# Kernel optimization log

Hardware: AMD Instinct MI355X
Metric: run time of the kernel (lower is better)

Reference implementation:

```python
import jax, jax.numpy as jnp
import numpy as np

N_NODES = 50000
N_EDGES = 800000
NUM_FEATS = 128
HIDDEN = 512
OUT = 2


def setup_inputs() -> dict:
    key = jax.random.key(0)
    k1, k2, k3, k4 = jax.random.split(key, 4)
    X = jax.random.normal(k1, (N_NODES, NUM_FEATS), dtype=jnp.float32)
    edge_index = jax.random.randint(k2, (2, N_EDGES), 0, N_NODES, dtype=jnp.int64)
    W1 = jax.random.normal(k3, (NUM_FEATS, HIDDEN), dtype=jnp.float32) / np.sqrt(NUM_FEATS)
    b1 = jnp.zeros((HIDDEN,), dtype=jnp.float32)
    W2 = jax.random.normal(k4, (HIDDEN, OUT), dtype=jnp.float32) / np.sqrt(HIDDEN)
    b2 = jnp.zeros((OUT,), dtype=jnp.float32)
    return {"X": X, "edge_index": edge_index, "W1": W1, "b1": b1, "W2": W2, "b2": b2}


def _gcn_conv(x, W, b, src, dst, dinv, n):
    # PyG GCNConv: x' = D^{-1/2} (A + I) D^{-1/2} (x W) + b
    xw = x @ W  # [N, C]
    edge_norm = dinv[src] * dinv[dst]  # [E]
    msg = xw[src] * edge_norm[:, None]  # [E, C] gathered messages
    agg = jax.ops.segment_sum(msg, dst, num_segments=n)
    agg = agg + xw * (dinv * dinv)[:, None]  # self-loop contribution
    return agg + b


def reference(X, edge_index, W1, b1, W2, b2):
    n = X.shape[0]
    src, dst = edge_index[0], edge_index[1]
    # degree with self-loops (gcn_norm): deg[i] = in_degree(i) + 1
    deg = jax.ops.segment_sum(jnp.ones_like(dst, dtype=X.dtype), dst, num_segments=n) + 1.0
    dinv = jax.lax.rsqrt(deg)
    h = jax.nn.relu(_gcn_conv(X, W1, b1, src, dst, dinv, n))
    logits = _gcn_conv(h, W2, b2, src, dst, dinv, n)
    # nn.Softmax() on a 2D tensor defaults to dim=1
    return jax.nn.softmax(logits, axis=1)
```

## Files before the change

### kernel.cpp

```cpp
#include <hip/hip_runtime.h>

#define N_FEATS 128
#define HIDDEN 512
#define NPAD 50176
#define NBKT 196
#define SLAB 4608
#define PA_EPB 4096
#define PA_BLOCKS 196
#define XQ_BLOCKS 3125

typedef __attribute__((ext_vector_type(4))) float floatx4;
typedef __attribute__((ext_vector_type(8))) short shortx8;

__device__ __forceinline__ unsigned short f2bf(float f) {
    union { float f; unsigned u; } a; a.f = f;
    unsigned r = a.u + 0x7fff + ((a.u >> 16) & 1);
    return (unsigned short)(r >> 16);
}

__global__ __launch_bounds__(256) void k_initA(const float* __restrict__ W1,
        unsigned short* __restrict__ w1t, const float* __restrict__ X,
        signed char* __restrict__ Xq, float* __restrict__ scale,
        const int* __restrict__ src, const int* __restrict__ dst,
        int* __restrict__ bcur, unsigned* __restrict__ staging, int E, int N) {
    int b = blockIdx.x, tid = threadIdx.x;
    if (b < PA_BLOCKS) {
        __shared__ int hist[NBKT];
        __shared__ int base[NBKT];
        for (int i = tid; i < NBKT; i += 256) hist[i] = 0;
        __syncthreads();
        #pragma unroll
        for (int i = 0; i < 4; ++i) {
            int e = b * PA_EPB + (i * 256 + tid) * 4;
            if (e + 3 < E) {
                int4 d4 = *reinterpret_cast<const int4*>(dst + e);
                atomicAdd(&hist[d4.x >> 8], 1);
                atomicAdd(&hist[d4.y >> 8], 1);
                atomicAdd(&hist[d4.z >> 8], 1);
                atomicAdd(&hist[d4.w >> 8], 1);
            } else {
                for (int k = 0; k < 4; ++k)
                    if (e + k < E) atomicAdd(&hist[dst[e + k] >> 8], 1);
            }
        }
        __syncthreads();
        for (int i = tid; i < NBKT; i += 256) {
            int c = hist[i];
            base[i] = c ? atomicAdd(&bcur[i], c) : 0;
            hist[i] = 0;
        }
        __syncthreads();
        #pragma unroll
        for (int i = 0; i < 4; ++i) {
            int e = b * PA_EPB + (i * 256 + tid) * 4;
            if (e + 3 < E) {
                int4 d4 = *reinterpret_cast<const int4*>(dst + e);
                int4 s4 = *reinterpret_cast<const int4*>(src + e);
                #define PUT(dd, ss) { int bk = (dd) >> 8; int r = atomicAdd(&hist[bk], 1); \
                    int pos = base[bk] + r; if (pos < SLAB) \
                    staging[(size_t)bk * SLAB + pos] = ((unsigned)(ss) << 8) | (unsigned)((dd) & 255); }
                PUT(d4.x, s4.x) PUT(d4.y, s4.y) PUT(d4.z, s4.z) PUT(d4.w, s4.w)
            } else {
                for (int k = 0; k < 4; ++k)
                    if (e + k < E) { int dd = dst[e + k], ss = src[e + k]; PUT(dd, ss) }
                #undef PUT
            }
        }
    } else if (b < PA_BLOCKS + 16) {
        __shared__ unsigned short t[64][65];
        int bb = b - PA_BLOCKS;
        int ki = bb >> 3, ni = bb & 7;
        #pragma unroll
        for (int i = 0; i < 16; ++i) {
            int idx = tid + i * 256;
            int r = idx >> 6, c = idx & 63;
            t[r][c] = f2bf(W1[(ki * 64 + r) * 512 + ni * 64 + c]);
        }
        __syncthreads();
        #pragma unroll
        for (int i = 0; i < 16; ++i) {
            int idx = tid + i * 256;
            int rn = idx >> 6, ck = idx & 63;
            w1t[(ni * 64 + rn) * 128 + ki * 64 + ck] = t[ck][rn];
        }
    } else {
        int r = (b - PA_BLOCKS - 16) * 16 + (tid >> 4);
        int lane = tid & 15;
        if (r < N) {
            const float* xp = X + (size_t)r * N_FEATS + lane * 8;
            float4 v0 = *reinterpret_cast<const float4*>(xp);
            float4 v1 = *reinterpret_cast<const float4*>(xp + 4);
            float f[8] = {v0.x, v0.y, v0.z, v0.w, v1.x, v1.y, v1.z, v1.w};
            float mx = 0.f;
            #pragma unroll
            for (int k = 0; k < 8; ++k) mx = fmaxf(mx, fabsf(f[k]));
            #pragma unroll
            for (int off = 1; off < 16; off <<= 1) mx = fmaxf(mx, __shfl_xor(mx, off));
            float rs = (mx > 0.f) ? 127.0f / mx : 0.f;
            union { signed char c[8]; uint2 u; } o;
            #pragma unroll
            for (int k = 0; k < 8; ++k) {
                int q = (int)rintf(f[k] * rs);
                q = q > 127 ? 127 : (q < -127 ? -127 : q);
                o.c[k] = (signed char)q;
            }
            *reinterpret_cast<uint2*>(Xq + (size_t)r * N_FEATS + lane * 8) = o.u;
            if (lane == 0) scale[r] = (mx > 0.f) ? mx / 127.0f : 0.f;
        }
    }
}

__global__ __launch_bounds__(256) void k_bucketB(const int* __restrict__ bcur,
        const unsigned* __restrict__ staging, const float* __restrict__ scale,
        int* __restrict__ csr_g, int* __restrict__ offs_g,
        int* __restrict__ cursor, float* __restrict__ dinvs, float* __restrict__ dscale) {
    __shared__ int hist[256];
    __shared__ int offs_l[256];
    __shared__ int sc[256];
    int b = blockIdx.x, tid = threadIdx.x;
    hist[tid] = 0;
    __syncthreads();
    int cnt = bcur[b];
    if (cnt > SLAB) cnt = SLAB;
    const unsigned* st = staging + (size_t)b * SLAB;
    for (int j = tid; j < cnt; j += 256) atomicAdd(&hist[st[j] & 255u], 1);
    __syncthreads();
    int c = hist[tid];
    sc[tid] = c;
    __syncthreads();
    #pragma unroll
    for (int off = 1; off < 256; off <<= 1) {
        int t = (tid >= off) ? sc[tid - off] : 0;
        __syncthreads();
        sc[tid] += t;
        __syncthreads();
    }
    int excl = sc[tid] - c;
    offs_l[tid] = excl;
    int node = (b << 8) + tid;
    float dv = rsqrtf((float)c + 1.0f);
    cursor[node] = c;
    dinvs[node] = dv;
    dscale[node] = dv * scale[node];
    offs_g[node] = b * SLAB + excl;
    hist[tid] = 0;
    __syncthreads();
    for (int j = tid; j < cnt; j += 256) {
        unsigned v = st[j];
        int dl = (int)(v & 255u);
        int s = (int)(v >> 8);
        int p = atomicAdd(&hist[dl], 1);
        csr_g[b * SLAB + offs_l[dl] + p] = s;
    }
}

__global__ __launch_bounds__(512, 4) void k_gather_gemm(
        const int* __restrict__ cursor, const float* __restrict__ dinvs,
        const float* __restrict__ dscale, const int* __restrict__ offs_g,
        const int* __restrict__ csr_g, const signed char* __restrict__ Xq,
        const unsigned short* __restrict__ w1t, const float* __restrict__ b1,
        const float* __restrict__ W2, float2* __restrict__ lps, int N) {
    __shared__ unsigned short As[128][136];
    __shared__ unsigned short Bs[128][136];
    __shared__ float b1s[HIDDEN];
    __shared__ float W2s[HIDDEN * 2];

    const int tid = threadIdx.x;
    const int m0 = blockIdx.x * 128;
    for (int i = tid; i < HIDDEN; i += 512) b1s[i] = b1[i];
    for (int i = tid; i < HIDDEN * 2; i += 512) W2s[i] = W2[i];

    union Q8 { uint2 u; signed char c[8]; };

    const int lane16 = tid & 15;
    const int nsub = tid >> 4;
    #pragma unroll
    for (int h = 0; h < 4; ++h) {
        int r = h * 32 + nsub;
        int gm = m0 + r;
        if (gm < N) {
            float dv = dinvs[gm];
            float ds = dscale[gm];
            int beg = offs_g[gm];
            int cnt = cursor[gm];
            const signed char* xrow = Xq + (size_t)gm * N_FEATS + lane16 * 8;
            Q8 sv; sv.u = *reinterpret_cast<const uint2*>(xrow);
            float a[8];
            #pragma unroll
            for (int k = 0; k < 8; ++k) a[k] = ds * (float)sv.c[k];
            const int* cp = csr_g + beg;
            int j = 0;
            int4 nxt;
            if (cnt >= 4) nxt = *reinterpret_cast<const int4*>(cp);
            for (; j + 4 <= cnt; j += 4) {
                int4 s4 = nxt;
                if (j + 8 <= cnt) nxt = *reinterpret_cast<const int4*>(cp + j + 4);
                float w0 = dscale[s4.x], w1 = dscale[s4.y], w2 = dscale[s4.z], w3 = dscale[s4.w];
                Q8 u0, u1, u2, u3;
                u0.u = *reinterpret_cast<const uint2*>(Xq + (size_t)s4.x * N_FEATS + lane16 * 8);
                u1.u = *reinterpret_cast<const uint2*>(Xq + (size_t)s4.y * N_FEATS + lane16 * 8);
                u2.u = *reinterpret_cast<const uint2*>(Xq + (size_t)s4.z * N_FEATS + lane16 * 8);
                u3.u = *reinterpret_cast<const uint2*>(Xq + (size_t)s4.w * N_FEATS + lane16 * 8);
                #pragma unroll
                for (int k = 0; k < 8; ++k)
                    a[k] += w0 * (float)u0.c[k] + w1 * (float)u1.c[k]
                          + w2 * (float)u2.c[k] + w3 * (float)u3.c[k];
            }
            for (; j < cnt; ++j) {
                int s = cp[j];
                float w = dscale[s];
                Q8 u; u.u = *reinterpret_cast<const uint2*>(Xq + (size_t)s * N_FEATS + lane16 * 8);
                #pragma unroll
                for (int k = 0; k < 8; ++k) a[k] += w * (float)u.c[k];
            }
            union { shortx8 v; unsigned short s[8]; } o;
            #pragma unroll
            for (int k = 0; k < 8; ++k) o.s[k] = f2bf(a[k] * dv);
            *reinterpret_cast<shortx8*>(&As[r][lane16 * 8]) = o.v;
        } else {
            shortx8 z = {0, 0, 0, 0, 0, 0, 0, 0};
            *reinterpret_cast<shortx8*>(&As[r][lane16 * 8]) = z;
        }
    }
    __syncthreads();

    const int wave = tid >> 6;
    const int lane64 = tid & 63;
    const int quad = lane64 >> 4;
    const int l16 = lane64 & 15;

    float accL0[4] = {0.f, 0.f, 0.f, 0.f};
    float accL1[4] = {0.f, 0.f, 0.f, 0.f};

    for (int n0 = 0; n0 < HIDDEN; n0 += 128) {
        #pragma unroll
        for (int it = 0; it < 4; ++it) {
            int flat = (tid + it * 512) * 8;
            int r = flat >> 7, c = flat & 127;
            *reinterpret_cast<shortx8*>(&Bs[r][c]) =
                *reinterpret_cast<const shortx8*>(w1t + (size_t)(n0 + r) * 128 + c);
        }
        __syncthreads();

        floatx4 acc[8];
        #pragma unroll
        for (int nt = 0; nt < 8; ++nt) acc[nt] = (floatx4){0.f, 0.f, 0.f, 0.f};

        #pragma unroll
        for (int ks = 0; ks < 4; ++ks) {
            shortx8 af = *reinterpret_cast<const shortx8*>(&As[wave * 16 + l16][ks * 32 + quad * 8]);
            #pragma unroll
            for (int nt = 0; nt < 8; ++nt) {
                shortx8 bf = *reinterpret_cast<const shortx8*>(&Bs[nt * 16 + l16][ks * 32 + quad * 8]);
                acc[nt] = __builtin_amdgcn_mfma_f32_16x16x32_bf16(af, bf, acc[nt], 0, 0, 0);
            }
        }

        #pragma unroll
        for (int nt = 0; nt < 8; ++nt) {
            int col = n0 + nt * 16 + l16;
            float bb = b1s[col];
            float w20 = W2s[col * 2 + 0];
            float w21 = W2s[col * 2 + 1];
            #pragma unroll
            for (int r = 0; r < 4; ++r) {
                float hh = acc[nt][r] + bb;
                hh = hh > 0.f ? hh : 0.f;
                accL0[r] += hh * w20;
                accL1[r] += hh * w21;
            }
        }
        __syncthreads();
    }

    #pragma unroll
    for (int off = 1; off < 16; off <<= 1) {
        #pragma unroll
        for (int r = 0; r < 4; ++r) {
            accL0[r] += __shfl_xor(accL0[r], off);
            accL1[r] += __shfl_xor(accL1[r], off);
        }
    }
    if (l16 == 0) {
        #pragma unroll
        for (int r = 0; r < 4; ++r) {
            int gm = m0 + wave * 16 + quad * 4 + r;
            if (gm < N) {
                float dv = dinvs[gm];
                lps[gm] = make_float2(dv * accL0[r], dv * accL1[r]);
            }
        }
    }
}

__global__ __launch_bounds__(256) void k_final(const int* __restrict__ cursor,
        const float* __restrict__ dinvs, const int* __restrict__ offs_g,
        const int* __restrict__ csr_g, const float2* __restrict__ lps,
        const float* __restrict__ b2, float* __restrict__ out, int N) {
    int t = blockIdx.x * 256 + threadIdx.x;
    int node = t >> 2;
    int lane = t & 3;
    if (node >= N) return;
    int cnt = cursor[node];
    int beg = offs_g[node];
    float a0 = 0.f, a1 = 0.f;
    for (int j = lane; j < cnt; j += 4) {
        float2 v = lps[csr_g[beg + j]];
        a0 += v.x;
        a1 += v.y;
    }
    #pragma unroll
    for (int off = 1; off < 4; off <<= 1) {
        a0 += __shfl_xor(a0, off);
        a1 += __shfl_xor(a1, off);
    }
    if (lane == 0) {
        float dv = dinvs[node];
        float2 self = lps[node];
        float l0 = dv * (a0 + self.x) + b2[0];
        float l1 = dv * (a1 + self.y) + b2[1];
        float m = fmaxf(l0, l1);
        float e0 = __expf(l0 - m), e1 = __expf(l1 - m);
        float inv = 1.0f / (e0 + e1);
        out[(size_t)node * 2 + 0] = e0 * inv;
        out[(size_t)node * 2 + 1] = e1 * inv;
    }
}

extern "C" void kernel_launch(void* const* d_in, const int* in_sizes, int n_in,
                              void* d_out, int out_size, void* d_ws, size_t ws_size,
                              hipStream_t stream) {
    const float* X  = (const float*)d_in[0];
    const int* ei   = (const int*)d_in[1];
    const float* W1 = (const float*)d_in[2];
    const float* b1 = (const float*)d_in[3];
    const float* W2 = (const float*)d_in[4];
    const float* b2 = (const float*)d_in[5];
    float* out = (float*)d_out;

    const int N = in_sizes[0] / N_FEATS;
    const int E = in_sizes[1] / 2;
    const int* src = ei;
    const int* dst = ei + E;

    int* cursor  = (int*)d_ws;
    int* bcur    = cursor + NPAD;
    int* offs_g  = bcur + 256;
    float* dinvs = (float*)(offs_g + NPAD);
    float* dscale = dinvs + NPAD;
    float* scale = dscale + NPAD;
    float2* lps  = (float2*)(scale + NPAD);
    unsigned short* w1t = (unsigned short*)(lps + NPAD);
    signed char* Xq = (signed char*)(w1t + 512 * 128);
    unsigned* staging = (unsigned*)(Xq + (size_t)NPAD * 128);
    int* csr_g   = (int*)(staging + (size_t)NBKT * SLAB);

    hipMemsetAsync(bcur, 0, 256 * sizeof(int), stream);
    k_initA      <<<PA_BLOCKS + 16 + XQ_BLOCKS, 256, 0, stream>>>(
                     W1, w1t, X, Xq, scale, src, dst, bcur, staging, E, N);
    k_bucketB    <<<NBKT, 256, 0, stream>>>(bcur, staging, scale, csr_g, offs_g,
                     cursor, dinvs, dscale);
    k_gather_gemm<<<NPAD / 128, 512, 0, stream>>>(cursor, dinvs, dscale, offs_g, csr_g,
                     Xq, w1t, b1, W2, lps, N);
    k_final      <<<((size_t)N * 4 + 255) / 256, 256, 0, stream>>>(
                     cursor, dinvs, offs_g, csr_g, lps, b2, out, N);
}
```

Measured before the change: 149.4 us.

## Split fused gather+GEMM into separate gather and MFMA GEMM kernels

The fused gather+GEMM kernel becomes two kernels. The first is a standalone gather that writes bf16 aggregated features to a global buffer, launched with many small blocks for better latency hiding. The second is a GEMM kernel that loads those rows into shared memory, with each wave now computing 32 rows using two MFMA accumulator sets. This aims to stop the irregular gather from stalling the MFMA phase in the same block, at the cost of an extra global write and read of the aggregated features (~12.8MB) and an additional kernel launch.

```diff
diff --git a/kernel.cpp b/kernel.cpp
--- a/kernel.cpp
+++ b/kernel.cpp
@@ -154,105 +154,114 @@
     }
 }
 
-__global__ __launch_bounds__(512, 4) void k_gather_gemm(
-        const int* __restrict__ cursor, const float* __restrict__ dinvs,
-        const float* __restrict__ dscale, const int* __restrict__ offs_g,
-        const int* __restrict__ csr_g, const signed char* __restrict__ Xq,
-        const unsigned short* __restrict__ w1t, const float* __restrict__ b1,
-        const float* __restrict__ W2, float2* __restrict__ lps, int N) {
+__global__ __launch_bounds__(256) void k_gather(const int* __restrict__ cursor,
+        const float* __restrict__ dinvs, const float* __restrict__ dscale,
+        const int* __restrict__ offs_g, const int* __restrict__ csr_g,
+        const signed char* __restrict__ Xq, unsigned short* __restrict__ aggAh, int N) {
+    int t = blockIdx.x * 256 + threadIdx.x;
+    int node = t >> 4;
+    int lane16 = t & 15;
+    if (node >= N) return;
+    union Q8 { uint2 u; signed char c[8]; };
+    float dv = dinvs[node];
+    float ds = dscale[node];
+    int beg = offs_g[node];
+    int cnt = cursor[node];
+    Q8 sv; sv.u = *reinterpret_cast<const uint2*>(Xq + (size_t)node * N_FEATS + lane16 * 8);
+    float a[8];
+    #pragma unroll
+    for (int k = 0; k < 8; ++k) a[k] = ds * (float)sv.c[k];
+    const int* cp = csr_g + beg;
+    int j = 0;
+    int4 nxt;
+    if (cnt >= 4) nxt = *reinterpret_cast<const int4*>(cp);
+    for (; j + 4 <= cnt; j += 4) {
+        int4 s4 = nxt;
+        if (j + 8 <= cnt) nxt = *reinterpret_cast<const int4*>(cp + j + 4);
+        float w0 = dscale[s4.x], w1 = dscale[s4.y], w2 = dscale[s4.z], w3 = dscale[s4.w];
+        Q8 u0, u1, u2, u3;
+        u0.u = *reinterpret_cast<const uint2*>(Xq + (size_t)s4.x * N_FEATS + lane16 * 8);
+        u1.u = *reinterpret_cast<const uint2*>(Xq + (size_t)s4.y * N_FEATS + lane16 * 8);
+        u2.u = *reinterpret_cast<const uint2*>(Xq + (size_t)s4.z * N_FEATS + lane16 * 8);
+        u3.u = *reinterpret_cast<const uint2*>(Xq + (size_t)s4.w * N_FEATS + lane16 * 8);
+        #pragma unroll
+        for (int k = 0; k < 8; ++k)
+            a[k] += w0 * (float)u0.c[k] + w1 * (float)u1.c[k]
+                  + w2 * (float)u2.c[k] + w3 * (float)u3.c[k];
+    }
+    for (; j < cnt; ++j) {
+        int s = cp[j];
+        float w = dscale[s];
+        Q8 u; u.u = *reinterpret_cast<const uint2*>(Xq + (size_t)s * N_FEATS + lane16 * 8);
+        #pragma unroll
+        for (int k = 0; k < 8; ++k) a[k] += w * (float)u.c[k];
+    }
+    union { shortx8 v; unsigned short s[8]; } o;
+    #pragma unroll
+    for (int k = 0; k < 8; ++k) o.s[k] = f2bf(a[k] * dv);
+    *reinterpret_cast<shortx8*>(aggAh + (size_t)node * N_FEATS + lane16 * 8) = o.v;
+}
+
+__global__ __launch_bounds__(256) void k_gemm(
+        const unsigned short* __restrict__ aggAh, const unsigned short* __restrict__ w1t,
+        const float* __restrict__ b1, const float* __restrict__ W2,
+        const float* __restrict__ dinvs, float2* __restrict__ lps, int N) {
     __shared__ unsigned short As[128][136];
     __shared__ unsigned short Bs[128][136];
     __shared__ float b1s[HIDDEN];
     __shared__ float W2s[HIDDEN * 2];
 
     const int tid = threadIdx.x;
+    const int wave = tid >> 6;
+    const int lane = tid & 63;
+    const int quad = lane >> 4;
+    const int l16 = lane & 15;
     const int m0 = blockIdx.x * 128;
-    for (int i = tid; i < HIDDEN; i += 512) b1s[i] = b1[i];
-    for (int i = tid; i < HIDDEN * 2; i += 512) W2s[i] = W2[i];
-
-    union Q8 { uint2 u; signed char c[8]; };
-
-    const int lane16 = tid & 15;
-    const int nsub = tid >> 4;
-    #pragma unroll
-    for (int h = 0; h < 4; ++h) {
-        int r = h * 32 + nsub;
+
+    for (int i = tid; i < HIDDEN; i += 256) b1s[i] = b1[i];
+    for (int i = tid; i < HIDDEN * 2; i += 256) W2s[i] = W2[i];
+
+    #pragma unroll
+    for (int it = 0; it < 8; ++it) {
+        int flat = (tid + it * 256) * 8;
+        int r = flat >> 7, c = flat & 127;
         int gm = m0 + r;
-        if (gm < N) {
-            float dv = dinvs[gm];
-            float ds = dscale[gm];
-            int beg = offs_g[gm];
-            int cnt = cursor[gm];
-            const signed char* xrow = Xq + (size_t)gm * N_FEATS + lane16 * 8;
-            Q8 sv; sv.u = *reinterpret_cast<const uint2*>(xrow);
-            float a[8];
-            #pragma unroll
-            for (int k = 0; k < 8; ++k) a[k] = ds * (float)sv.c[k];
-            const int* cp = csr_g + beg;
-            int j = 0;
-            int4 nxt;
-            if (cnt >= 4) nxt = *reinterpret_cast<const int4*>(cp);
-            for (; j + 4 <= cnt; j += 4) {
-                int4 s4 = nxt;
-                if (j + 8 <= cnt) nxt = *reinterpret_cast<const int4*>(cp + j + 4);
-                float w0 = dscale[s4.x], w1 = dscale[s4.y], w2 = dscale[s4.z], w3 = dscale[s4.w];
-                Q8 u0, u1, u2, u3;
-                u0.u = *reinterpret_cast<const uint2*>(Xq + (size_t)s4.x * N_FEATS + lane16 * 8);
-                u1.u = *reinterpret_cast<const uint2*>(Xq + (size_t)s4.y * N_FEATS + lane16 * 8);
-                u2.u = *reinterpret_cast<const uint2*>(Xq + (size_t)s4.z * N_FEATS + lane16 * 8);
-                u3.u = *reinterpret_cast<const uint2*>(Xq + (size_t)s4.w * N_FEATS + lane16 * 8);
-                #pragma unroll
-                for (int k = 0; k < 8; ++k)
-                    a[k] += w0 * (float)u0.c[k] + w1 * (float)u1.c[k]
-                          + w2 * (float)u2.c[k] + w3 * (float)u3.c[k];
-            }
-            for (; j < cnt; ++j) {
-                int s = cp[j];
-                float w = dscale[s];
-                Q8 u; u.u = *reinterpret_cast<const uint2*>(Xq + (size_t)s * N_FEATS + lane16 * 8);
-                #pragma unroll
-                for (int k = 0; k < 8; ++k) a[k] += w * (float)u.c[k];
-            }
-            union { shortx8 v; unsigned short s[8]; } o;
-            #pragma unroll
-            for (int k = 0; k < 8; ++k) o.s[k] = f2bf(a[k] * dv);
-            *reinterpret_cast<shortx8*>(&As[r][lane16 * 8]) = o.v;
-        } else {
-            shortx8 z = {0, 0, 0, 0, 0, 0, 0, 0};
-            *reinterpret_cast<shortx8*>(&As[r][lane16 * 8]) = z;
-        }
-    }
-    __syncthreads();
-
-    const int wave = tid >> 6;
-    const int lane64 = tid & 63;
-    const int quad = lane64 >> 4;
-    const int l16 = lane64 & 15;
-
-    float accL0[4] = {0.f, 0.f, 0.f, 0.f};
-    float accL1[4] = {0.f, 0.f, 0.f, 0.f};
+        shortx8 v = {0, 0, 0, 0, 0, 0, 0, 0};
+        if (gm < N) v = *reinterpret_cast<const shortx8*>(aggAh + (size_t)gm * 128 + c);
+        *reinterpret_cast<shortx8*>(&As[r][c]) = v;
+    }
+
+    float accL0[2][4], accL1[2][4];
+    #pragma unroll
+    for (int s = 0; s < 2; ++s)
+        #pragma unroll
+        for (int r = 0; r < 4; ++r) { accL0[s][r] = 0.f; accL1[s][r] = 0.f; }
 
     for (int n0 = 0; n0 < HIDDEN; n0 += 128) {
         #pragma unroll
-        for (int it = 0; it < 4; ++it) {
-            int flat = (tid + it * 512) * 8;
+        for (int it = 0; it < 8; ++it) {
+            int flat = (tid + it * 256) * 8;
             int r = flat >> 7, c = flat & 127;
             *reinterpret_cast<shortx8*>(&Bs[r][c]) =
                 *reinterpret_cast<const shortx8*>(w1t + (size_t)(n0 + r) * 128 + c);
         }
         __syncthreads();
 
-        floatx4 acc[8];
-        #pragma unroll
-        for (int nt = 0; nt < 8; ++nt) acc[nt] = (floatx4){0.f, 0.f, 0.f, 0.f};
+        floatx4 acc[2][8];
+        #pragma unroll
+        for (int s = 0; s < 2; ++s)
+            #pragma unroll
+            for (int nt = 0; nt < 8; ++nt) acc[s][nt] = (floatx4){0.f, 0.f, 0.f, 0.f};
 
         #pragma unroll
         for (int ks = 0; ks < 4; ++ks) {
-            shortx8 af = *reinterpret_cast<const shortx8*>(&As[wave * 16 + l16][ks * 32 + quad * 8]);
+            shortx8 af0 = *reinterpret_cast<const shortx8*>(&As[wave * 32 + l16][ks * 32 + quad * 8]);
+            shortx8 af1 = *reinterpret_cast<const shortx8*>(&As[wave * 32 + 16 + l16][ks * 32 + quad * 8]);
             #pragma unroll
             for (int nt = 0; nt < 8; ++nt) {
                 shortx8 bf = *reinterpret_cast<const shortx8*>(&Bs[nt * 16 + l16][ks * 32 + quad * 8]);
-                acc[nt] = __builtin_amdgcn_mfma_f32_16x16x32_bf16(af, bf, acc[nt], 0, 0, 0);
+                acc[0][nt] = __builtin_amdgcn_mfma_f32_16x16x32_bf16(af0, bf, acc[0][nt], 0, 0, 0);
+                acc[1][nt] = __builtin_amdgcn_mfma_f32_16x16x32_bf16(af1, bf, acc[1][nt], 0, 0, 0);
             }
         }
 
@@ -263,33 +272,40 @@
             float w20 = W2s[col * 2 + 0];
             float w21 = W2s[col * 2 + 1];
             #pragma unroll
+            for (int s = 0; s < 2; ++s) {
+                #pragma unroll
+                for (int r = 0; r < 4; ++r) {
+                    float h = acc[s][nt][r] + bb;
+                    h = h > 0.f ? h : 0.f;
+                    accL0[s][r] += h * w20;
+                    accL1[s][r] += h * w21;
+                }
+            }
+        }
+        __syncthreads();
+    }
+
+    #pragma unroll
+    for (int off = 1; off < 16; off <<= 1) {
+        #pragma unroll
+        for (int s = 0; s < 2; ++s)
+            #pragma unroll
             for (int r = 0; r < 4; ++r) {
-                float hh = acc[nt][r] + bb;
-                hh = hh > 0.f ? hh : 0.f;
-                accL0[r] += hh * w20;
-                accL1[r] += hh * w21;
-            }
-        }
-        __syncthreads();
-    }
-
-    #pragma unroll
-    for (int off = 1; off < 16; off <<= 1) {
-        #pragma unroll
-        for (int r = 0; r < 4; ++r) {
-            accL0[r] += __shfl_xor(accL0[r], off);
-            accL1[r] += __shfl_xor(accL1[r], off);
-        }
+                accL0[s][r] += __shfl_xor(accL0[s][r], off);
+                accL1[s][r] += __shfl_xor(accL1[s][r], off);
+            }
     }
     if (l16 == 0) {
         #pragma unroll
-        for (int r = 0; r < 4; ++r) {
-            int gm = m0 + wave * 16 + quad * 4 + r;
-            if (gm < N) {
-                float dv = dinvs[gm];
-                lps[gm] = make_float2(dv * accL0[r], dv * accL1[r]);
-            }
-        }
+        for (int s = 0; s < 2; ++s)
+            #pragma unroll
+            for (int r = 0; r < 4; ++r) {
+                int gm = m0 + wave * 32 + s * 16 + quad * 4 + r;
+                if (gm < N) {
+                    float dv = dinvs[gm];
+                    lps[gm] = make_float2(dv * accL0[s][r], dv * accL1[s][r]);
+                }
+            }
     }
 }
 
@@ -354,14 +370,16 @@
     signed char* Xq = (signed char*)(w1t + 512 * 128);
     unsigned* staging = (unsigned*)(Xq + (size_t)NPAD * 128);
     int* csr_g   = (int*)(staging + (size_t)NBKT * SLAB);
+    unsigned short* aggAh = (unsigned short*)(csr_g + (size_t)NBKT * SLAB);
 
     hipMemsetAsync(bcur, 0, 256 * sizeof(int), stream);
-    k_initA      <<<PA_BLOCKS + 16 + XQ_BLOCKS, 256, 0, stream>>>(
-                     W1, w1t, X, Xq, scale, src, dst, bcur, staging, E, N);
-    k_bucketB    <<<NBKT, 256, 0, stream>>>(bcur, staging, scale, csr_g, offs_g,
-                     cursor, dinvs, dscale);
-    k_gather_gemm<<<NPAD / 128, 512, 0, stream>>>(cursor, dinvs, dscale, offs_g, csr_g,
-                     Xq, w1t, b1, W2, lps, N);
-    k_final      <<<((size_t)N * 4 + 255) / 256, 256, 0, stream>>>(
-                     cursor, dinvs, offs_g, csr_g, lps, b2, out, N);
-}
+    k_initA  <<<PA_BLOCKS + 16 + XQ_BLOCKS, 256, 0, stream>>>(
+                 W1, w1t, X, Xq, scale, src, dst, bcur, staging, E, N);
+    k_bucketB<<<NBKT, 256, 0, stream>>>(bcur, staging, scale, csr_g, offs_g,
+                 cursor, dinvs, dscale);
+    k_gather <<<(N * 16 + 255) / 256, 256, 0, stream>>>(cursor, dinvs, dscale,
+                 offs_g, csr_g, Xq, aggAh, N);
+    k_gemm   <<<NPAD / 128, 256, 0, stream>>>(aggAh, w1t, b1, W2, dinvs, lps, N);
+    k_final  <<<((size_t)N * 4 + 255) / 256, 256, 0, stream>>>(
+                 cursor, dinvs, offs_g, csr_g, lps, b2, out, N);
+}
```

After: 158.6 us. 1.06x slower.

## Store quantized X as biased uint8 and prefetch W1 tiles during epilogue

Applied to the files above, without the earlier changes.

Quantized features are now stored as unsigned bytes offset by 127. Each byte is extracted with a shift and mask, and the offset is removed once per row by subtracting 127 times the accumulated edge weights. This avoids sign-extension work in the gather inner loop. The first W1 tile is also loaded before the gather phase, and each later tile is loaded after the MFMA loop so the global load overlaps the bias/ReLU/W2 epilogue. The cost is an extra weight accumulator per row, and the bias subtraction may lose a little float precision.

```diff
diff --git a/kernel.cpp b/kernel.cpp
--- a/kernel.cpp
+++ b/kernel.cpp
@@ -17,10 +17,11 @@
     unsigned r = a.u + 0x7fff + ((a.u >> 16) & 1);
     return (unsigned short)(r >> 16);
 }
+#define CV(w, s) ((float)(((w) >> (s)) & 255u))
 
 __global__ __launch_bounds__(256) void k_initA(const float* __restrict__ W1,
         unsigned short* __restrict__ w1t, const float* __restrict__ X,
-        signed char* __restrict__ Xq, float* __restrict__ scale,
+        unsigned char* __restrict__ Xq, float* __restrict__ scale,
         const int* __restrict__ src, const int* __restrict__ dst,
         int* __restrict__ bcur, unsigned* __restrict__ staging, int E, int N) {
     int b = blockIdx.x, tid = threadIdx.x;
@@ -97,12 +98,12 @@
             #pragma unroll
             for (int off = 1; off < 16; off <<= 1) mx = fmaxf(mx, __shfl_xor(mx, off));
             float rs = (mx > 0.f) ? 127.0f / mx : 0.f;
-            union { signed char c[8]; uint2 u; } o;
+            union { unsigned char c[8]; uint2 u; } o;
             #pragma unroll
             for (int k = 0; k < 8; ++k) {
                 int q = (int)rintf(f[k] * rs);
                 q = q > 127 ? 127 : (q < -127 ? -127 : q);
-                o.c[k] = (signed char)q;
+                o.c[k] = (unsigned char)(q + 127);
             }
             *reinterpret_cast<uint2*>(Xq + (size_t)r * N_FEATS + lane * 8) = o.u;
             if (lane == 0) scale[r] = (mx > 0.f) ? mx / 127.0f : 0.f;
@@ -157,7 +158,7 @@
 __global__ __launch_bounds__(512, 4) void k_gather_gemm(
         const int* __restrict__ cursor, const float* __restrict__ dinvs,
         const float* __restrict__ dscale, const int* __restrict__ offs_g,
-        const int* __restrict__ csr_g, const signed char* __restrict__ Xq,
+        const int* __restrict__ csr_g, const unsigned char* __restrict__ Xq,
         const unsigned short* __restrict__ w1t, const float* __restrict__ b1,
         const float* __restrict__ W2, float2* __restrict__ lps, int N) {
     __shared__ unsigned short As[128][136];
@@ -170,7 +171,13 @@
     for (int i = tid; i < HIDDEN; i += 512) b1s[i] = b1[i];
     for (int i = tid; i < HIDDEN * 2; i += 512) W2s[i] = W2[i];
 
-    union Q8 { uint2 u; signed char c[8]; };
+    #pragma unroll
+    for (int it = 0; it < 4; ++it) {
+        int flat = (tid + it * 512) * 8;
+        int r = flat >> 7, c = flat & 127;
+        *reinterpret_cast<shortx8*>(&Bs[r][c]) =
+            *reinterpret_cast<const shortx8*>(w1t + (size_t)r * 128 + c);
+    }
 
     const int lane16 = tid & 15;
     const int nsub = tid >> 4;
@@ -183,11 +190,13 @@
             float ds = dscale[gm];
             int beg = offs_g[gm];
             int cnt = cursor[gm];
-            const signed char* xrow = Xq + (size_t)gm * N_FEATS + lane16 * 8;
-            Q8 sv; sv.u = *reinterpret_cast<const uint2*>(xrow);
+            uint2 sv = *reinterpret_cast<const uint2*>(Xq + (size_t)gm * N_FEATS + lane16 * 8);
+            float wacc = ds;
             float a[8];
-            #pragma unroll
-            for (int k = 0; k < 8; ++k) a[k] = ds * (float)sv.c[k];
+            a[0] = ds * CV(sv.x, 0);  a[1] = ds * CV(sv.x, 8);
+            a[2] = ds * CV(sv.x, 16); a[3] = ds * CV(sv.x, 24);
+            a[4] = ds * CV(sv.y, 0);  a[5] = ds * CV(sv.y, 8);
+            a[6] = ds * CV(sv.y, 16); a[7] = ds * CV(sv.y, 24);
             const int* cp = csr_g + beg;
             int j = 0;
             int4 nxt;
@@ -196,26 +205,34 @@
                 int4 s4 = nxt;
                 if (j + 8 <= cnt) nxt = *reinterpret_cast<const int4*>(cp + j + 4);
                 float w0 = dscale[s4.x], w1 = dscale[s4.y], w2 = dscale[s4.z], w3 = dscale[s4.w];
-                Q8 u0, u1, u2, u3;
-                u0.u = *reinterpret_cast<const uint2*>(Xq + (size_t)s4.x * N_FEATS + lane16 * 8);
-                u1.u = *reinterpret_cast<const uint2*>(Xq + (size_t)s4.y * N_FEATS + lane16 * 8);
-                u2.u = *reinterpret_cast<const uint2*>(Xq + (size_t)s4.z * N_FEATS + lane16 * 8);
-                u3.u = *reinterpret_cast<const uint2*>(Xq + (size_t)s4.w * N_FEATS + lane16 * 8);
-                #pragma unroll
-                for (int k = 0; k < 8; ++k)
-                    a[k] += w0 * (float)u0.c[k] + w1 * (float)u1.c[k]
-                          + w2 * (float)u2.c[k] + w3 * (float)u3.c[k];
+                uint2 u0 = *reinterpret_cast<const uint2*>(Xq + (size_t)s4.x * N_FEATS + lane16 * 8);
+                uint2 u1 = *reinterpret_cast<const uint2*>(Xq + (size_t)s4.y * N_FEATS + lane16 * 8);
+                uint2 u2 = *reinterpret_cast<const uint2*>(Xq + (size_t)s4.z * N_FEATS + lane16 * 8);
+                uint2 u3 = *reinterpret_cast<const uint2*>(Xq + (size_t)s4.w * N_FEATS + lane16 * 8);
+                wacc += w0 + w1 + w2 + w3;
+                a[0] += w0 * CV(u0.x, 0)  + w1 * CV(u1.x, 0)  + w2 * CV(u2.x, 0)  + w3 * CV(u3.x, 0);
+                a[1] += w0 * CV(u0.x, 8)  + w1 * CV(u1.x, 8)  + w2 * CV(u2.x, 8)  + w3 * CV(u3.x, 8);
+                a[2] += w0 * CV(u0.x, 16) + w1 * CV(u1.x, 16) + w2 * CV(u2.x, 16) + w3 * CV(u3.x, 16);
+                a[3] += w0 * CV(u0.x, 24) + w1 * CV(u1.x, 24) + w2 * CV(u2.x, 24) + w3 * CV(u3.x, 24);
+                a[4] += w0 * CV(u0.y, 0)  + w1 * CV(u1.y, 0)  + w2 * CV(u2.y, 0)  + w3 * CV(u3.y, 0);
+                a[5] += w0 * CV(u0.y, 8)  + w1 * CV(u1.y, 8)  + w2 * CV(u2.y, 8)  + w3 * CV(u3.y, 8);
+                a[6] += w0 * CV(u0.y, 16) + w1 * CV(u1.y, 16) + w2 * CV(u2.y, 16) + w3 * CV(u3.y, 16);
+                a[7] += w0 * CV(u0.y, 24) + w1 * CV(u1.y, 24) + w2 * CV(u2.y, 24) + w3 * CV(u3.y, 24);
             }
             for (; j < cnt; ++j) {
                 int s = cp[j];
                 float w = dscale[s];
-                Q8 u; u.u = *reinterpret_cast<const uint2*>(Xq + (size_t)s * N_FEATS + lane16 * 8);
-                #pragma unroll
-                for (int k = 0; k < 8; ++k) a[k] += w * (float)u.c[k];
-            }
+                uint2 u = *reinterpret_cast<const uint2*>(Xq + (size_t)s * N_FEATS + lane16 * 8);
+                wacc += w;
+                a[0] += w * CV(u.x, 0);  a[1] += w * CV(u.x, 8);
+                a[2] += w * CV(u.x, 16); a[3] += w * CV(u.x, 24);
+                a[4] += w * CV(u.y, 0);  a[5] += w * CV(u.y, 8);
+                a[6] += w * CV(u.y, 16); a[7] += w * CV(u.y, 24);
+            }
+            float c127 = 127.0f * wacc;
             union { shortx8 v; unsigned short s[8]; } o;
             #pragma unroll
-            for (int k = 0; k < 8; ++k) o.s[k] = f2bf(a[k] * dv);
+            for (int k = 0; k < 8; ++k) o.s[k] = f2bf((a[k] - c127) * dv);
             *reinterpret_cast<shortx8*>(&As[r][lane16 * 8]) = o.v;
         } else {
             shortx8 z = {0, 0, 0, 0, 0, 0, 0, 0};
@@ -232,16 +249,8 @@
     float accL0[4] = {0.f, 0.f, 0.f, 0.f};
     float accL1[4] = {0.f, 0.f, 0.f, 0.f};
 
-    for (int n0 = 0; n0 < HIDDEN; n0 += 128) {
-        #pragma unroll
-        for (int it = 0; it < 4; ++it) {
-            int flat = (tid + it * 512) * 8;
-            int r = flat >> 7, c = flat & 127;
-            *reinterpret_cast<shortx8*>(&Bs[r][c]) =
-                *reinterpret_cast<const shortx8*>(w1t + (size_t)(n0 + r) * 128 + c);
-        }
-        __syncthreads();
-
+    for (int ch = 0; ch < 4; ++ch) {
+        int n0 = ch * 128;
         floatx4 acc[8];
         #pragma unroll
         for (int nt = 0; nt < 8; ++nt) acc[nt] = (floatx4){0.f, 0.f, 0.f, 0.f};
@@ -253,6 +262,17 @@
             for (int nt = 0; nt < 8; ++nt) {
                 shortx8 bf = *reinterpret_cast<const shortx8*>(&Bs[nt * 16 + l16][ks * 32 + quad * 8]);
                 acc[nt] = __builtin_amdgcn_mfma_f32_16x16x32_bf16(af, bf, acc[nt], 0, 0, 0);
+            }
+        }
+        __syncthreads();
+
+        if (ch < 3) {
+            #pragma unroll
+            for (int it = 0; it < 4; ++it) {
+                int flat = (tid + it * 512) * 8;
+                int r = flat >> 7, c = flat & 127;
+                *reinterpret_cast<shortx8*>(&Bs[r][c]) =
+                    *reinterpret_cast<const shortx8*>(w1t + (size_t)(n0 + 128 + r) * 128 + c);
             }
         }
 
@@ -270,7 +290,7 @@
                 accL1[r] += hh * w21;
             }
         }
-        __syncthreads();
+        if (ch < 3) __syncthreads();
     }
 
     #pragma unroll
@@ -351,7 +371,7 @@
     float* scale = dscale + NPAD;
     float2* lps  = (float2*)(scale + NPAD);
     unsigned short* w1t = (unsigned short*)(lps + NPAD);
-    signed char* Xq = (signed char*)(w1t + 512 * 128);
+    unsigned char* Xq = (unsigned char*)(w1t + 512 * 128);
     unsigned* staging = (unsigned*)(Xq + (size_t)NPAD * 128);
     int* csr_g   = (int*)(staging + (size_t)NBKT * SLAB);
 
```

New measurement: 150.5 us. About the same (+0.7%).
